# Optimization experiments

Hardware: AMD Instinct MI355X
Metric: run time of the kernel (lower is better)

The kernel has to match this reference:

```python
import jax, jax.numpy as jnp
import numpy as np

N_NODES = 200000
N_EDGES = 400000
N_GRAPHS = 8192
N_LAYERS = 4
HID = 256
BN_EPS = 1e-5


def setup_inputs() -> dict:
    key = jax.random.key(0)
    ks = jax.random.split(key, 10)
    s = lambda fan_in: 1.0 / np.sqrt(fan_in)
    return {
        "x": jax.random.normal(ks[0], (N_NODES, 14), jnp.float32),
        "edge_attr": jax.random.normal(ks[1], (N_EDGES, 3), jnp.float32),
        "edge_index": jax.random.randint(ks[2], (2, N_EDGES), 0, N_NODES, jnp.int64),
        "batch": jnp.sort(jax.random.randint(ks[3], (N_NODES,), 0, N_GRAPHS, jnp.int64)),
        "in_W": jax.random.normal(ks[4], (14, HID), jnp.float32) * s(14),
        "in_b": jnp.zeros((HID,), jnp.float32),
        "edge_W": jax.random.normal(ks[5], (N_LAYERS, 3, HID), jnp.float32) * s(3),
        "edge_b": jnp.zeros((N_LAYERS, HID), jnp.float32),
        "w1": jax.random.normal(ks[6], (N_LAYERS, HID, HID), jnp.float32) * s(HID),
        "b1": jnp.zeros((N_LAYERS, HID), jnp.float32),
        "w2": jax.random.normal(ks[7], (N_LAYERS, HID, HID), jnp.float32) * s(HID),
        "b2": jnp.zeros((N_LAYERS, HID), jnp.float32),
        "gamma": jnp.ones((N_LAYERS, HID), jnp.float32),
        "beta": jnp.zeros((N_LAYERS, HID), jnp.float32),
    }


def reference(x, edge_attr, edge_index, batch, in_W, in_b, edge_W, edge_b,
              w1, b1, w2, b2, gamma, beta):
    n_nodes = x.shape[0]
    src, dst = edge_index[0], edge_index[1]

    h = x @ in_W + in_b  # [N, HID] input projection

    for l in range(N_LAYERS):
        # GINEConv message: relu(x_j + Lin(edge_attr)), aggregated by sum at dst
        e = edge_attr @ edge_W[l] + edge_b[l]          # [E, HID]
        m = jax.nn.relu(h[src] + e)                    # gather + add + relu
        agg = jax.ops.segment_sum(m, dst, num_segments=n_nodes)
        # (1 + eps) * x_i + agg, eps = 0 (default, not trainable)
        z = h + agg
        # 2-layer MLP
        z = jax.nn.relu(z @ w1[l] + b1[l]) @ w2[l] + b2[l]
        # BatchNorm1d (training-mode batch statistics, biased variance)
        mu = z.mean(axis=0)
        var = z.var(axis=0)
        z = (z - mu) * jax.lax.rsqrt(var + BN_EPS) * gamma[l] + beta[l]
        h = jax.nn.relu(z)

    # dropout is identity at inference; global_mean_pool over graphs
    sums = jax.ops.segment_sum(h, batch, num_segments=N_GRAPHS)
    counts = jax.ops.segment_sum(jnp.ones((n_nodes,), h.dtype), batch,
                                 num_segments=N_GRAPHS)
    return sums / jnp.maximum(counts, 1.0)[:, None]
```

## Files before the change

### kernel.cpp

```cpp
#include <hip/hip_runtime.h>

#define HID 256
typedef unsigned short bfb;
typedef _Float16 f16x8_t __attribute__((ext_vector_type(8)));
typedef __attribute__((ext_vector_type(4))) float f32x4_t;

__device__ inline float bfb2f(bfb u) {
  _Float16 h;
  __builtin_memcpy(&h, &u, 2);
  return (float)h;
}
__device__ inline bfb f2bfb(float f) {
  _Float16 h = (_Float16)f;
  bfb u;
  __builtin_memcpy(&u, &h, 2);
  return u;
}
__device__ inline float ldf(const bfb* p, size_t i) { return bfb2f(p[i]); }
__device__ inline void stf(bfb* p, size_t i, float v) { p[i] = f2bfb(v); }

__device__ inline void gld16(const void* g, void* l) {
  __builtin_amdgcn_global_load_lds(
      (const __attribute__((address_space(1))) void*)g,
      (__attribute__((address_space(3))) void*)l, 16, 0, 0);
}
__device__ inline f32x4_t mfma16(f16x8_t a, f16x8_t b, f32x4_t c) {
  return __builtin_amdgcn_mfma_f32_16x16x32_f16(a, b, c, 0, 0, 0);
}

__global__ __launch_bounds__(256) void k_prep_w(
    const float* __restrict__ w1, const float* __restrict__ w2,
    bfb* __restrict__ wbuf, int n_layers) {
  int t = blockIdx.x * 256 + threadIdx.x;
  int total = n_layers * 2 * 65536;
  if (t >= total) return;
  int l = t / 131072;
  int rem = t - l * 131072;
  int which = rem >> 16;
  int e = rem & 65535;
  int r = e & 7;
  int lane = (e >> 3) & 63;
  int g = (e >> 9) & 7;
  int nt = e >> 12;
  int n = nt * 16 + (lane & 15);
  int k = g * 32 + ((lane >> 4) & 3) * 8 + r;
  const float* src = (which ? w2 : w1) + (size_t)l * 65536;
  bfb* dst = wbuf + (size_t)l * 131072 + (size_t)which * 65536;
  dst[e] = f2bfb(src[k * 256 + n]);
}

__global__ __launch_bounds__(256) void k_input_proj(
    const float* __restrict__ x, const float* __restrict__ W,
    const float* __restrict__ bias, bfb* __restrict__ z, int n_nodes) {
  __shared__ float sW[14 * HID];
  __shared__ float sx[64 * 14];
  for (int i = threadIdx.x; i < 14 * HID; i += blockDim.x) sW[i] = W[i];
  int c = threadIdx.x;
  float b = bias[c];
  int n0 = blockIdx.x * 64;
  int nmax = min(n0 + 64, n_nodes);
  int cnt = (nmax - n0) * 14;
  for (int i = threadIdx.x; i < cnt; i += blockDim.x) sx[i] = x[(size_t)n0 * 14 + i];
  __syncthreads();
  for (int n = n0; n < nmax; n++) {
    const float* xr = &sx[(n - n0) * 14];
    float acc = b;
#pragma unroll
    for (int k = 0; k < 14; k++) acc = fmaf(xr[k], sW[k * HID + c], acc);
    stf(z, (size_t)n * HID + c, acc);
  }
}

__global__ __launch_bounds__(256) void k_hist(const int* __restrict__ dsts,
                                              int* deg, int ne) {
  int e = blockIdx.x * 256 + threadIdx.x;
  if (e < ne) atomicAdd(&deg[dsts[e]], 1);
}

__global__ __launch_bounds__(256) void k_scan1(const int* __restrict__ deg,
                                               int* bsum, int n) {
  __shared__ int sd[256];
  int i0 = blockIdx.x * 1024 + threadIdx.x * 4;
  int s = 0;
#pragma unroll
  for (int j = 0; j < 4; j++) {
    int i = i0 + j;
    if (i < n) s += deg[i];
  }
  sd[threadIdx.x] = s;
  __syncthreads();
  for (int off = 128; off > 0; off >>= 1) {
    if (threadIdx.x < off) sd[threadIdx.x] += sd[threadIdx.x + off];
    __syncthreads();
  }
  if (threadIdx.x == 0) bsum[blockIdx.x] = sd[0];
}

__global__ __launch_bounds__(256) void k_scan2(int* bsum, int nb) {
  __shared__ int sd[256];
  __shared__ int stot;
  int tid = threadIdx.x;
  int carry = 0;
  for (int base = 0; base < nb; base += 256) {
    int v = (base + tid < nb) ? bsum[base + tid] : 0;
    sd[tid] = v;
    __syncthreads();
    for (int off = 1; off < 256; off <<= 1) {
      int t = (tid >= off) ? sd[tid - off] : 0;
      __syncthreads();
      sd[tid] += t;
      __syncthreads();
    }
    int incl = sd[tid];
    if (base + tid < nb) bsum[base + tid] = carry + incl - v;
    if (tid == 255) stot = incl;
    __syncthreads();
    carry += stot;
    __syncthreads();
  }
}

__global__ __launch_bounds__(256) void k_scan3(const int* __restrict__ deg,
                                               const int* __restrict__ bsum,
                                               int* row_start, int* cursor, int n) {
  __shared__ int sd[256];
  int tid = threadIdx.x;
  int i0 = blockIdx.x * 1024 + tid * 4;
  int d[4];
  int s = 0;
#pragma unroll
  for (int j = 0; j < 4; j++) {
    int i = i0 + j;
    d[j] = (i < n) ? deg[i] : 0;
    s += d[j];
  }
  sd[tid] = s;
  __syncthreads();
  for (int off = 1; off < 256; off <<= 1) {
    int t = (tid >= off) ? sd[tid - off] : 0;
    __syncthreads();
    sd[tid] += t;
    __syncthreads();
  }
  int excl = sd[tid] - s + bsum[blockIdx.x];
#pragma unroll
  for (int j = 0; j < 4; j++) {
    int i = i0 + j;
    if (i < n) {
      row_start[i] = excl;
      cursor[i] = excl;
      if (i == n - 1) row_start[n] = excl + d[j];
      excl += d[j];
    }
  }
}

__global__ __launch_bounds__(256) void k_fill(
    const int* __restrict__ dsts, const int* __restrict__ srcs,
    const float* __restrict__ ea, int* cursor,
    int* __restrict__ src_s, float4* __restrict__ ea_s, int ne) {
  int e = blockIdx.x * 256 + threadIdx.x;
  if (e < ne) {
    int p = atomicAdd(&cursor[dsts[e]], 1);
    src_s[p] = srcs[e];
    ea_s[p] = make_float4(ea[(size_t)e * 3], ea[(size_t)e * 3 + 1],
                          ea[(size_t)e * 3 + 2], 0.0f);
  }
}

template <int BN>
__global__ __launch_bounds__(256) void k_aggregate(
    const bfb* __restrict__ zin, const float4* __restrict__ ea_s,
    const int* __restrict__ src_s, const int* __restrict__ row_start,
    const float* __restrict__ eW, const float* __restrict__ eb,
    const float* __restrict__ stats, bfb* __restrict__ zout, int n_nodes) {
  __shared__ float sw0[HID], sw1[HID], sw2[HID], sb[HID], ssc[HID], ssh[HID];
  int tid = threadIdx.x;
  sw0[tid] = eW[tid];
  sw1[tid] = eW[HID + tid];
  sw2[tid] = eW[2 * HID + tid];
  sb[tid] = eb[tid];
  if (BN) {
    ssc[tid] = stats[2 * HID + tid];
    ssh[tid] = stats[3 * HID + tid];
  }
  __syncthreads();
  int w = tid >> 6, lane = tid & 63;
  int n = blockIdx.x * 4 + w;
  if (n >= n_nodes) return;
  int c0 = lane * 4;
  float w0[4], w1[4], w2[4], bb[4], sc[4], sh[4];
#pragma unroll
  for (int j = 0; j < 4; j++) {
    w0[j] = sw0[c0 + j]; w1[j] = sw1[c0 + j]; w2[j] = sw2[c0 + j]; bb[j] = sb[c0 + j];
    if (BN) { sc[j] = ssc[c0 + j]; sh[j] = ssh[c0 + j]; }
  }
  int i = row_start[n], i1 = row_start[n + 1];
  ushort4 hv = *(const ushort4*)&zin[(size_t)n * HID + c0];
  float hvf[4] = {bfb2f(hv.x), bfb2f(hv.y), bfb2f(hv.z), bfb2f(hv.w)};
  float acc[4];
#pragma unroll
  for (int j = 0; j < 4; j++)
    acc[j] = BN ? fmaxf(fmaf(hvf[j], sc[j], sh[j]), 0.0f) : hvf[j];
  for (; i + 2 <= i1; i += 2) {
    int s0 = src_s[i], s1 = src_s[i + 1];
    float4 a0 = ea_s[i];
    float4 a1 = ea_s[i + 1];
    ushort4 sv0 = *(const ushort4*)&zin[(size_t)s0 * HID + c0];
    ushort4 sv1 = *(const ushort4*)&zin[(size_t)s1 * HID + c0];
    float h0[4] = {bfb2f(sv0.x), bfb2f(sv0.y), bfb2f(sv0.z), bfb2f(sv0.w)};
    float h1[4] = {bfb2f(sv1.x), bfb2f(sv1.y), bfb2f(sv1.z), bfb2f(sv1.w)};
#pragma unroll
    for (int j = 0; j < 4; j++) {
      float e0 = fmaf(a0.x, w0[j], fmaf(a0.y, w1[j], fmaf(a0.z, w2[j], bb[j])));
      float e1 = fmaf(a1.x, w0[j], fmaf(a1.y, w1[j], fmaf(a1.z, w2[j], bb[j])));
      float g0 = BN ? fmaxf(fmaf(h0[j], sc[j], sh[j]), 0.0f) : h0[j];
      float g1 = BN ? fmaxf(fmaf(h1[j], sc[j], sh[j]), 0.0f) : h1[j];
      acc[j] += fmaxf(g0 + e0, 0.0f);
      acc[j] += fmaxf(g1 + e1, 0.0f);
    }
  }
  if (i < i1) {
    int s0 = src_s[i];
    float4 a0 = ea_s[i];
    ushort4 sv0 = *(const ushort4*)&zin[(size_t)s0 * HID + c0];
    float h0[4] = {bfb2f(sv0.x), bfb2f(sv0.y), bfb2f(sv0.z), bfb2f(sv0.w)};
#pragma unroll
    for (int j = 0; j < 4; j++) {
      float e0 = fmaf(a0.x, w0[j], fmaf(a0.y, w1[j], fmaf(a0.z, w2[j], bb[j])));
      float g0 = BN ? fmaxf(fmaf(h0[j], sc[j], sh[j]), 0.0f) : h0[j];
      acc[j] += fmaxf(g0 + e0, 0.0f);
    }
  }
  ushort4 o;
  o.x = f2bfb(acc[0]); o.y = f2bfb(acc[1]); o.z = f2bfb(acc[2]); o.w = f2bfb(acc[3]);
  *(ushort4*)&zout[(size_t)n * HID + c0] = o;
}

template <int RELU, int STATS>
__global__ __launch_bounds__(512, 2) void k_gemm_mfma(
    const bfb* __restrict__ A, const bfb* __restrict__ Wp,
    const float* __restrict__ bias, bfb* __restrict__ C,
    int Mreal, float* __restrict__ stats) {
  __shared__ __align__(16) bfb smem[16384];
  int tid = threadIdx.x;
  int lane = tid & 63, wid = tid >> 6;
  int l15 = lane & 15, lq = lane >> 4;
  size_t bm = (size_t)blockIdx.x * 64;

#pragma unroll
  for (int p = 0; p < 4; p++) {
    int b = p * 8192 + tid * 16;
    int row = b >> 9;
    int off = b & 511;
    int src = (off ^ ((row & 7) << 4)) >> 1;
    gld16(A + (bm + row) * 256 + src, (char*)smem + b);
  }

  f16x8_t wf[2][8];
#pragma unroll
  for (int ni = 0; ni < 2; ni++)
#pragma unroll
    for (int g = 0; g < 8; g++)
      wf[ni][g] = *(const f16x8_t*)(
          Wp + ((size_t)((wid * 2 + ni) * 8 + g) * 64 + lane) * 8);

  __syncthreads();

  f32x4_t acc[4][2] = {};
  const char* As = (const char*)smem;
#pragma unroll
  for (int g = 0; g < 8; g++) {
    f16x8_t af[4];
#pragma unroll
    for (int mi = 0; mi < 4; mi++) {
      int row = mi * 16 + l15;
      int kb = g * 64 + lq * 16;
      af[mi] = *(const f16x8_t*)(As + row * 512 + (kb ^ ((row & 7) << 4)));
    }
#pragma unroll
    for (int ni = 0; ni < 2; ni++)
#pragma unroll
      for (int mi = 0; mi < 4; mi++)
        acc[mi][ni] = mfma16(af[mi], wf[ni][g], acc[mi][ni]);
  }
  __syncthreads();

  char* Cs = (char*)smem;
  int crow0 = lq * 4;
  int ccol0 = wid * 32 + l15;
  float ssum[2] = {}, ssq[2] = {};
#pragma unroll
  for (int ni = 0; ni < 2; ni++) {
    int col = ccol0 + ni * 16;
    float b = bias[col];
#pragma unroll
    for (int mi = 0; mi < 4; mi++) {
#pragma unroll
      for (int r = 0; r < 4; r++) {
        int row = mi * 16 + crow0 + r;
        float v = acc[mi][ni][r] + b;
        if (RELU) v = fmaxf(v, 0.0f);
        int byte = (row * 512 + col * 2) ^ ((row & 15) << 4);
        *(bfb*)(Cs + byte) = f2bfb(v);
        if (STATS && (int)bm + row < Mreal) {
          ssum[ni] += v;
          ssq[ni] = fmaf(v, v, ssq[ni]);
        }
      }
    }
  }
  if (STATS) {
#pragma unroll
    for (int ni = 0; ni < 2; ni++) {
      float s = ssum[ni], q = ssq[ni];
      s += __shfl_xor(s, 16); s += __shfl_xor(s, 32);
      q += __shfl_xor(q, 16); q += __shfl_xor(q, 32);
      if (lq == 0) {
        int col = ccol0 + ni * 16;
        atomicAdd(&stats[col], s);
        atomicAdd(&stats[HID + col], q);
      }
    }
  }
  __syncthreads();
  {
    char* Cg = (char*)(C + bm * 256);
#pragma unroll
    for (int j = 0; j < 4; j++) {
      int b = j * 8192 + tid * 16;
      int row = b >> 9;
      int off = b & 511;
      float4 v = *(const float4*)(Cs + (row << 9) + (off ^ ((row & 15) << 4)));
      *(float4*)(Cg + b) = v;
    }
  }
}

__global__ __launch_bounds__(256) void k_bn_finalize(
    float* stats, const float* __restrict__ gamma, const float* __restrict__ beta,
    float inv_n) {
  int c = threadIdx.x;
  float mu = stats[c] * inv_n;
  float var = stats[HID + c] * inv_n - mu * mu;
  float sc = gamma[c] * rsqrtf(var + 1e-5f);
  stats[2 * HID + c] = sc;
  stats[3 * HID + c] = beta[c] - mu * sc;
  stats[c] = 0.0f;
  stats[HID + c] = 0.0f;
}

__global__ __launch_bounds__(256) void k_pool(
    const bfb* __restrict__ z, const float* __restrict__ stats,
    const int* __restrict__ batch, float* out, int n_nodes, int npb) {
  int c = threadIdx.x;
  float sc = stats[2 * HID + c];
  float sh = stats[3 * HID + c];
  int n0 = blockIdx.x * npb;
  int n1 = min(n0 + npb, n_nodes);
  if (n0 >= n1) return;
  int cur = batch[n0];
  float acc = 0.0f;
  for (int n = n0; n < n1; n++) {
    int g = batch[n];
    if (g != cur) {
      atomicAdd(&out[(size_t)cur * HID + c], acc);
      acc = 0.0f;
      cur = g;
    }
    acc += fmaxf(fmaf(ldf(z, (size_t)n * HID + c), sc, sh), 0.0f);
  }
  atomicAdd(&out[(size_t)cur * HID + c], acc);
}

__global__ __launch_bounds__(256) void k_div(
    float* out, const int* __restrict__ batch, int n_nodes) {
  int g = blockIdx.x;
  int lo = 0, hi = n_nodes;
  while (lo < hi) {
    int mid = (lo + hi) >> 1;
    if (batch[mid] < g) lo = mid + 1; else hi = mid;
  }
  int lo2 = lo, hi2 = n_nodes;
  while (lo2 < hi2) {
    int mid = (lo2 + hi2) >> 1;
    if (batch[mid] < g + 1) lo2 = mid + 1; else hi2 = mid;
  }
  float cnt = (float)(lo2 - lo);
  float inv = 1.0f / fmaxf(cnt, 1.0f);
  out[(size_t)g * HID + threadIdx.x] *= inv;
}

extern "C" void kernel_launch(void* const* d_in, const int* in_sizes, int n_in,
                              void* d_out, int out_size, void* d_ws, size_t ws_size,
                              hipStream_t stream) {
  const float* x = (const float*)d_in[0];
  const float* edge_attr = (const float*)d_in[1];
  const int* edge_index = (const int*)d_in[2];
  const int* batch = (const int*)d_in[3];
  const float* in_W = (const float*)d_in[4];
  const float* in_b = (const float*)d_in[5];
  const float* edge_W = (const float*)d_in[6];
  const float* edge_b = (const float*)d_in[7];
  const float* w1 = (const float*)d_in[8];
  const float* b1 = (const float*)d_in[9];
  const float* w2 = (const float*)d_in[10];
  const float* b2 = (const float*)d_in[11];
  const float* gamma = (const float*)d_in[12];
  const float* beta = (const float*)d_in[13];
  float* out = (float*)d_out;

  int n_nodes = in_sizes[3];
  int n_edges = in_sizes[1] / 3;
  int n_graphs = out_size / HID;
  int n_layers = in_sizes[7] / HID;

  const int* srcs = edge_index;
  const int* dsts = edge_index + n_edges;

  int Mp = ((n_nodes + 127) / 128) * 128;
  size_t nhp = (size_t)Mp * HID;

  char* ws = (char*)d_ws;
  size_t off = 0;
  float* stats = (float*)(ws + off); off += 4096;
  bfb* wbuf = (bfb*)(ws + off); off += (size_t)n_layers * 131072 * 2;
  int* deg = (int*)(ws + off); off += ((size_t)n_nodes * 4 + 255) & ~255ull;
  int* row_start = (int*)(ws + off); off += ((size_t)(n_nodes + 1) * 4 + 255) & ~255ull;
  int* cursor = (int*)(ws + off); off += ((size_t)n_nodes * 4 + 255) & ~255ull;
  int* bsum = (int*)(ws + off); off += 4096;
  int* src_s = (int*)(ws + off); off += ((size_t)n_edges * 4 + 255) & ~255ull;
  float4* ea_s = (float4*)(ws + off); off += (size_t)n_edges * 16;
  bfb* P0 = (bfb*)(ws + off); off += nhp * 2;
  bfb* P1 = (bfb*)(ws + off);

  hipMemsetAsync(out, 0, (size_t)out_size * sizeof(float), stream);
  hipMemsetAsync(deg, 0, (size_t)n_nodes * 4, stream);
  hipMemsetAsync(stats, 0, 4096, stream);

  k_prep_w<<<(n_layers * 131072 + 255) / 256, 256, 0, stream>>>(w1, w2, wbuf, n_layers);
  k_input_proj<<<(n_nodes + 63) / 64, 256, 0, stream>>>(x, in_W, in_b, P0, n_nodes);

  int np = (n_nodes + 1023) / 1024;
  k_hist<<<(n_edges + 255) / 256, 256, 0, stream>>>(dsts, deg, n_edges);
  k_scan1<<<np, 256, 0, stream>>>(deg, bsum, n_nodes);
  k_scan2<<<1, 256, 0, stream>>>(bsum, np);
  k_scan3<<<np, 256, 0, stream>>>(deg, bsum, row_start, cursor, n_nodes);
  k_fill<<<(n_edges + 255) / 256, 256, 0, stream>>>(dsts, srcs, edge_attr, cursor,
                                                    src_s, ea_s, n_edges);

  bfb* cur = P0;
  bfb* oth = P1;
  int gagg = (n_nodes + 3) / 4;
  int gemm_grid = Mp / 64;
  for (int l = 0; l < n_layers; l++) {
    if (l == 0)
      k_aggregate<0><<<gagg, 256, 0, stream>>>(
          cur, ea_s, src_s, row_start, edge_W + (size_t)l * 3 * HID,
          edge_b + (size_t)l * HID, stats, oth, n_nodes);
    else
      k_aggregate<1><<<gagg, 256, 0, stream>>>(
          cur, ea_s, src_s, row_start, edge_W + (size_t)l * 3 * HID,
          edge_b + (size_t)l * HID, stats, oth, n_nodes);
    bfb* wl = wbuf + (size_t)l * 131072;
    k_gemm_mfma<1, 0><<<gemm_grid, 512, 0, stream>>>(
        oth, wl, b1 + (size_t)l * HID, cur, n_nodes, nullptr);
    k_gemm_mfma<0, 1><<<gemm_grid, 512, 0, stream>>>(
        cur, wl + 65536, b2 + (size_t)l * HID, oth, n_nodes, stats);
    k_bn_finalize<<<1, 256, 0, stream>>>(stats, gamma + (size_t)l * HID,
                                         beta + (size_t)l * HID, 1.0f / (float)n_nodes);
    bfb* t = cur; cur = oth; oth = t;
  }

  k_pool<<<(n_nodes + 31) / 32, 256, 0, stream>>>(cur, stats, batch, out, n_nodes, 32);
  k_div<<<n_graphs, 256, 0, stream>>>(out, batch, n_nodes);
}
```

Measured before the change: 1.039 ms.

## Fuse the two MLP GEMMs into one kernel keeping the hidden tile in LDS

Merges the two per-layer GEMM launches into a single kernel. The ReLU'd first-layer output tile is written back into shared memory and consumed directly by the second GEMM, which avoids a global round trip of the intermediate activation and one launch per layer. Weight fragments are now loaded from global memory inside the k-loop instead of being preloaded into registers, which lowers register pressure but exposes that load latency. The ping-pong buffer swap is removed, so output goes to cur and the next layer's aggregate reads it from there.

After: 935.9 us. 1.11x faster.

```diff
diff --git a/kernel.cpp b/kernel.cpp
--- a/kernel.cpp
+++ b/kernel.cpp
@@ -237,10 +237,10 @@
   *(ushort4*)&zout[(size_t)n * HID + c0] = o;
 }
 
-template <int RELU, int STATS>
-__global__ __launch_bounds__(512, 2) void k_gemm_mfma(
-    const bfb* __restrict__ A, const bfb* __restrict__ Wp,
-    const float* __restrict__ bias, bfb* __restrict__ C,
+__global__ __launch_bounds__(512, 2) void k_mlp4(
+    const bfb* __restrict__ A, const bfb* __restrict__ Wp1,
+    const bfb* __restrict__ Wp2, const float* __restrict__ b1,
+    const float* __restrict__ b2, bfb* __restrict__ C,
     int Mreal, float* __restrict__ stats) {
   __shared__ __align__(16) bfb smem[16384];
   int tid = threadIdx.x;
@@ -256,19 +256,11 @@
     int src = (off ^ ((row & 7) << 4)) >> 1;
     gld16(A + (bm + row) * 256 + src, (char*)smem + b);
   }
-
-  f16x8_t wf[2][8];
-#pragma unroll
-  for (int ni = 0; ni < 2; ni++)
-#pragma unroll
-    for (int g = 0; g < 8; g++)
-      wf[ni][g] = *(const f16x8_t*)(
-          Wp + ((size_t)((wid * 2 + ni) * 8 + g) * 64 + lane) * 8);
-
   __syncthreads();
 
   f32x4_t acc[4][2] = {};
   const char* As = (const char*)smem;
+
 #pragma unroll
   for (int g = 0; g < 8; g++) {
     f16x8_t af[4];
@@ -279,10 +271,50 @@
       af[mi] = *(const f16x8_t*)(As + row * 512 + (kb ^ ((row & 7) << 4)));
     }
 #pragma unroll
-    for (int ni = 0; ni < 2; ni++)
+    for (int ni = 0; ni < 2; ni++) {
+      f16x8_t wf = *(const f16x8_t*)(
+          Wp1 + ((size_t)((wid * 2 + ni) * 8 + g) * 64 + lane) * 8);
 #pragma unroll
       for (int mi = 0; mi < 4; mi++)
-        acc[mi][ni] = mfma16(af[mi], wf[ni][g], acc[mi][ni]);
+        acc[mi][ni] = mfma16(af[mi], wf, acc[mi][ni]);
+    }
+  }
+  __syncthreads();
+
+#pragma unroll
+  for (int ni = 0; ni < 2; ni++) {
+    int col = wid * 32 + ni * 16 + l15;
+    float b = b1[col];
+#pragma unroll
+    for (int mi = 0; mi < 4; mi++)
+#pragma unroll
+      for (int r = 0; r < 4; r++) {
+        int row = mi * 16 + lq * 4 + r;
+        float v = fmaxf(acc[mi][ni][r] + b, 0.0f);
+        int byte = row * 512 + ((col * 2) ^ ((row & 7) << 4));
+        *(bfb*)((char*)smem + byte) = f2bfb(v);
+        acc[mi][ni][r] = 0.0f;
+      }
+  }
+  __syncthreads();
+
+#pragma unroll
+  for (int g = 0; g < 8; g++) {
+    f16x8_t af[4];
+#pragma unroll
+    for (int mi = 0; mi < 4; mi++) {
+      int row = mi * 16 + l15;
+      int kb = g * 64 + lq * 16;
+      af[mi] = *(const f16x8_t*)(As + row * 512 + (kb ^ ((row & 7) << 4)));
+    }
+#pragma unroll
+    for (int ni = 0; ni < 2; ni++) {
+      f16x8_t wf = *(const f16x8_t*)(
+          Wp2 + ((size_t)((wid * 2 + ni) * 8 + g) * 64 + lane) * 8);
+#pragma unroll
+      for (int mi = 0; mi < 4; mi++)
+        acc[mi][ni] = mfma16(af[mi], wf, acc[mi][ni]);
+    }
   }
   __syncthreads();
 
@@ -293,34 +325,31 @@
 #pragma unroll
   for (int ni = 0; ni < 2; ni++) {
     int col = ccol0 + ni * 16;
-    float b = bias[col];
+    float b = b2[col];
 #pragma unroll
     for (int mi = 0; mi < 4; mi++) {
 #pragma unroll
       for (int r = 0; r < 4; r++) {
         int row = mi * 16 + crow0 + r;
         float v = acc[mi][ni][r] + b;
-        if (RELU) v = fmaxf(v, 0.0f);
         int byte = (row * 512 + col * 2) ^ ((row & 15) << 4);
         *(bfb*)(Cs + byte) = f2bfb(v);
-        if (STATS && (int)bm + row < Mreal) {
+        if ((int)bm + row < Mreal) {
           ssum[ni] += v;
           ssq[ni] = fmaf(v, v, ssq[ni]);
         }
       }
     }
   }
-  if (STATS) {
-#pragma unroll
-    for (int ni = 0; ni < 2; ni++) {
-      float s = ssum[ni], q = ssq[ni];
-      s += __shfl_xor(s, 16); s += __shfl_xor(s, 32);
-      q += __shfl_xor(q, 16); q += __shfl_xor(q, 32);
-      if (lq == 0) {
-        int col = ccol0 + ni * 16;
-        atomicAdd(&stats[col], s);
-        atomicAdd(&stats[HID + col], q);
-      }
+#pragma unroll
+  for (int ni = 0; ni < 2; ni++) {
+    float s = ssum[ni], q = ssq[ni];
+    s += __shfl_xor(s, 16); s += __shfl_xor(s, 32);
+    q += __shfl_xor(q, 16); q += __shfl_xor(q, 32);
+    if (lq == 0) {
+      int col = ccol0 + ni * 16;
+      atomicAdd(&stats[col], s);
+      atomicAdd(&stats[HID + col], q);
     }
   }
   __syncthreads();
@@ -463,13 +492,11 @@
           cur, ea_s, src_s, row_start, edge_W + (size_t)l * 3 * HID,
           edge_b + (size_t)l * HID, stats, oth, n_nodes);
     bfb* wl = wbuf + (size_t)l * 131072;
-    k_gemm_mfma<1, 0><<<gemm_grid, 512, 0, stream>>>(
-        oth, wl, b1 + (size_t)l * HID, cur, n_nodes, nullptr);
-    k_gemm_mfma<0, 1><<<gemm_grid, 512, 0, stream>>>(
-        cur, wl + 65536, b2 + (size_t)l * HID, oth, n_nodes, stats);
+    k_mlp4<<<gemm_grid, 512, 0, stream>>>(
+        oth, wl, wl + 65536, b1 + (size_t)l * HID, b2 + (size_t)l * HID,
+        cur, n_nodes, stats);
     k_bn_finalize<<<1, 256, 0, stream>>>(stats, gamma + (size_t)l * HID,
                                          beta + (size_t)l * HID, 1.0f / (float)n_nodes);
-    bfb* t = cur; cur = oth; oth = t;
   }
 
   k_pool<<<(n_nodes + 31) / 32, 256, 0, stream>>>(cur, stats, batch, out, n_nodes, 32);
```
